# Kernel optimization log

Measured on AMD Instinct MI355X. Metric: run time of the kernel, lower is better.

Reference implementation:

```python
import jax, jax.numpy as jnp
import numpy as np

B, S, HID = 2, 1024, 2048
HQ, HKV, HD = 32, 8, 64
ROPE_BASE = 10000.0

def _rope_tables(seq_len, head_dim):
    inv_freq = 1.0 / (ROPE_BASE ** (np.arange(0, head_dim, 2, dtype=np.float32) / head_dim))
    t = np.arange(seq_len, dtype=np.float32)
    freqs = np.outer(t, inv_freq)                      # [S, d/2]
    emb = np.concatenate([freqs, freqs], axis=-1)      # [S, d]
    return jnp.asarray(np.cos(emb)), jnp.asarray(np.sin(emb))

def setup_inputs() -> dict:
    key = jax.random.key(0)
    ks = jax.random.split(key, 5)
    cos, sin = _rope_tables(S, HD)
    return {
        'hidden_states': jax.random.normal(ks[0], (B, S, HID), jnp.float32),
        'cos': cos, 'sin': sin,
        'Wq': jax.random.normal(ks[1], (HID, HID), jnp.float32) * (HID ** -0.5),
        'Wk': jax.random.normal(ks[2], (HID, HKV * HD), jnp.float32) * (HID ** -0.5),
        'Wv': jax.random.normal(ks[3], (HID, HKV * HD), jnp.float32) * (HID ** -0.5),
        'Wo': jax.random.normal(ks[4], (HID, HID), jnp.float32) * (HID ** -0.5),
    }

def _rotate_half(x):
    d = x.shape[-1]
    return jnp.concatenate([-x[..., d // 2:], x[..., :d // 2]], axis=-1)

def reference(hidden_states, cos, sin, Wq, Wk, Wv, Wo):
    b, s, _ = hidden_states.shape
    q = (hidden_states @ Wq).reshape(b, s, HQ, HD)    # [b,s,Hq,d]
    k = (hidden_states @ Wk).reshape(b, s, HKV, HD)   # [b,s,Hkv,d]
    v = (hidden_states @ Wv).reshape(b, s, HKV, HD)
    # RoPE: cos/sin [s,d] broadcast as [s,1,d] over head dim
    c = cos[:, None, :]
    sn = sin[:, None, :]
    q = q * c + _rotate_half(q) * sn
    k = k * c + _rotate_half(k) * sn
    # GQA: expand kv heads to query heads (repeat_kv)
    n_rep = HQ // HKV
    k = jnp.repeat(k, n_rep, axis=2)                  # [b,s,Hq,d]
    v = jnp.repeat(v, n_rep, axis=2)
    scale = HD ** -0.5
    scores = jnp.einsum('bqhd,bkhd->bhqk', q, k) * scale  # [b,Hq,s,s]
    causal = jnp.tril(jnp.ones((s, s), bool))
    scores = jnp.where(causal, scores, jnp.float32(-1e30))
    probs = jax.nn.softmax(scores.astype(jnp.float32), axis=-1).astype(q.dtype)
    out = jnp.einsum('bhqk,bkhd->bqhd', probs, v).reshape(b, s, HID)
    return out @ Wo
```

## Files before the change

### kernel.cpp

```cpp
#include <hip/hip_runtime.h>
#include <math.h>

#define B_   2
#define S_   1024
#define HID_ 2048
#define HQ_  32
#define HKV_ 8
#define HD_  64
#define NQKV 3072

using short8  = __attribute__((ext_vector_type(8))) short;
using floatx4 = __attribute__((ext_vector_type(4))) float;

__device__ __forceinline__ unsigned short f2bf(float x) {
    unsigned int u = __builtin_bit_cast(unsigned int, x);
    u += 0x7FFFu + ((u >> 16) & 1u);
    return (unsigned short)(u >> 16);
}
__device__ __forceinline__ float bf2f(unsigned short u) {
    return __builtin_bit_cast(float, (unsigned int)u << 16);
}

__device__ __forceinline__ void gl_lds16(const unsigned short* g, unsigned short* l) {
    __builtin_amdgcn_global_load_lds(
        (const __attribute__((address_space(1))) void*)g,
        (__attribute__((address_space(3))) void*)l, 16, 0, 0);
}

__global__ __launch_bounds__(256) void gemm_qkv(const unsigned short* __restrict__ A,
                                                const unsigned short* __restrict__ Bt,
                                                unsigned short* __restrict__ Qp,
                                                unsigned short* __restrict__ KVp) {
    __shared__ __align__(16) unsigned short As[128 * 32];
    __shared__ __align__(16) unsigned short Bs[128 * 32];

    int bid = blockIdx.x;
    int m0, n0, z, Nw, nc0;
    unsigned short* C;
    if (bid < 512) {
        n0 = (bid & 15) * 128; m0 = ((bid >> 4) & 15) * 128; z = bid >> 8;
        C = Qp + (size_t)z * 2048 * 2048; Nw = 2048; nc0 = n0;
    } else {
        bid -= 512;
        n0 = 2048 + (bid & 7) * 128; m0 = ((bid >> 3) & 15) * 128; z = bid >> 7;
        C = KVp + (size_t)z * 2048 * 1024; Nw = 1024; nc0 = n0 - 2048;
    }
    const int kbase = z * 1024;

    const int tid  = threadIdx.x;
    const int w    = tid >> 6;
    const int lane = tid & 63;
    const int col  = lane & 15;
    const int quad = lane >> 4;
    const int wm = (w >> 1) * 64;
    const int wn = (w & 1) * 64;

    const int srow = lane >> 2;
    const int skof = (lane & 3) * 8;
    const unsigned short* Ag = A  + (size_t)(m0 + srow) * HID_ + skof;
    const unsigned short* Bg = Bt + (size_t)(n0 + srow) * HID_ + skof;
    const int rb = w * 16;

    floatx4 acc[4][4] = {};

    for (int k0 = kbase; k0 < kbase + 1024; k0 += 32) {
        gl_lds16(Ag + (size_t)(rb     ) * HID_ + k0, &As[(rb     ) * 32]);
        gl_lds16(Ag + (size_t)(rb + 64) * HID_ + k0, &As[(rb + 64) * 32]);
        gl_lds16(Bg + (size_t)(rb     ) * HID_ + k0, &Bs[(rb     ) * 32]);
        gl_lds16(Bg + (size_t)(rb + 64) * HID_ + k0, &Bs[(rb + 64) * 32]);
        __syncthreads();

        short8 af[4], bfr[4];
#pragma unroll
        for (int i = 0; i < 4; ++i)
            af[i] = *(const short8*)&As[(wm + i * 16 + col) * 32 + quad * 8];
#pragma unroll
        for (int j = 0; j < 4; ++j)
            bfr[j] = *(const short8*)&Bs[(wn + j * 16 + col) * 32 + quad * 8];
#pragma unroll
        for (int i = 0; i < 4; ++i)
#pragma unroll
            for (int j = 0; j < 4; ++j)
                acc[i][j] = __builtin_amdgcn_mfma_f32_16x16x32_bf16(
                    af[i], bfr[j], acc[i][j], 0, 0, 0);
        __syncthreads();
    }

#pragma unroll
    for (int i = 0; i < 4; ++i)
#pragma unroll
        for (int j = 0; j < 4; ++j)
#pragma unroll
            for (int r = 0; r < 4; ++r)
                C[(size_t)(m0 + wm + i * 16 + quad * 4 + r) * Nw
                  + (nc0 + wn + j * 16 + col)] = f2bf(acc[i][j][r]);
}

__global__ __launch_bounds__(256) void gemm_wo(const unsigned short* __restrict__ A,
                                               const unsigned short* __restrict__ Bt,
                                               float* __restrict__ Cf,
                                               unsigned short* __restrict__ Cp1) {
    __shared__ __align__(16) unsigned short As[128 * 32];
    __shared__ __align__(16) unsigned short Bs[128 * 32];

    const int m0 = blockIdx.y * 128;
    const int n0 = blockIdx.x * 128;
    const int z  = blockIdx.z;
    const int kbase = z * 1024;

    const int tid  = threadIdx.x;
    const int w    = tid >> 6;
    const int lane = tid & 63;
    const int col  = lane & 15;
    const int quad = lane >> 4;
    const int wm = (w >> 1) * 64;
    const int wn = (w & 1) * 64;

    const int srow = lane >> 2;
    const int skof = (lane & 3) * 8;
    const unsigned short* Ag = A  + (size_t)(m0 + srow) * HID_ + skof;
    const unsigned short* Bg = Bt + (size_t)(n0 + srow) * HID_ + skof;
    const int rb = w * 16;

    floatx4 acc[4][4] = {};

    for (int k0 = kbase; k0 < kbase + 1024; k0 += 32) {
        gl_lds16(Ag + (size_t)(rb     ) * HID_ + k0, &As[(rb     ) * 32]);
        gl_lds16(Ag + (size_t)(rb + 64) * HID_ + k0, &As[(rb + 64) * 32]);
        gl_lds16(Bg + (size_t)(rb     ) * HID_ + k0, &Bs[(rb     ) * 32]);
        gl_lds16(Bg + (size_t)(rb + 64) * HID_ + k0, &Bs[(rb + 64) * 32]);
        __syncthreads();

        short8 af[4], bfr[4];
#pragma unroll
        for (int i = 0; i < 4; ++i)
            af[i] = *(const short8*)&As[(wm + i * 16 + col) * 32 + quad * 8];
#pragma unroll
        for (int j = 0; j < 4; ++j)
            bfr[j] = *(const short8*)&Bs[(wn + j * 16 + col) * 32 + quad * 8];
#pragma unroll
        for (int i = 0; i < 4; ++i)
#pragma unroll
            for (int j = 0; j < 4; ++j)
                acc[i][j] = __builtin_amdgcn_mfma_f32_16x16x32_bf16(
                    af[i], bfr[j], acc[i][j], 0, 0, 0);
        __syncthreads();
    }

#pragma unroll
    for (int i = 0; i < 4; ++i)
#pragma unroll
        for (int j = 0; j < 4; ++j)
#pragma unroll
            for (int r = 0; r < 4; ++r) {
                size_t off = (size_t)(m0 + wm + i * 16 + quad * 4 + r) * HID_
                           + (n0 + wn + j * 16 + col);
                if (z == 0) Cf[off] = acc[i][j][r];
                else        Cp1[off] = f2bf(acc[i][j][r]);
            }
}

__global__ __launch_bounds__(256) void reduce_wo(float* __restrict__ out,
                                                 const unsigned short* __restrict__ p1) {
    int i4 = (blockIdx.x * 256 + threadIdx.x) * 4;
    float4 o = *(float4*)&out[i4];
    ushort4 p = *(const ushort4*)&p1[i4];
    o.x += bf2f(p.x); o.y += bf2f(p.y); o.z += bf2f(p.z); o.w += bf2f(p.w);
    *(float4*)&out[i4] = o;
}

__global__ __launch_bounds__(256) void convert_x(const float* __restrict__ in,
                                                 unsigned short* __restrict__ out) {
    int tid = blockIdx.x * 256 + threadIdx.x;
    float4 v = *(const float4*)&in[(size_t)tid * 4];
    ushort4 o = {f2bf(v.x), f2bf(v.y), f2bf(v.z), f2bf(v.w)};
    *(ushort4*)&out[(size_t)tid * 4] = o;
}

__global__ __launch_bounds__(256) void transpose_qkv(const float* __restrict__ Wq,
                                                     const float* __restrict__ Wk,
                                                     const float* __restrict__ Wv,
                                                     unsigned short* __restrict__ WcatT) {
    __shared__ float tile[32][33];
    int bid = blockIdx.x;
    const float* W;
    unsigned short* WT;
    int N, tn0, tk0;
    if (bid < 4096) {
        W = Wq; WT = WcatT; N = HID_;
        tn0 = (bid & 63) * 32; tk0 = (bid >> 6) * 32;
    } else if (bid < 5120) {
        bid -= 4096;
        W = Wk; WT = WcatT + (size_t)HID_ * HID_; N = 512;
        tn0 = (bid & 15) * 32; tk0 = (bid >> 4) * 32;
    } else {
        bid -= 5120;
        W = Wv; WT = WcatT + (size_t)(HID_ + 512) * HID_; N = 512;
        tn0 = (bid & 15) * 32; tk0 = (bid >> 4) * 32;
    }
    const int r  = threadIdx.x >> 3;
    const int c4 = (threadIdx.x & 7) * 4;
    float4 v = *(const float4*)&W[(size_t)(tk0 + r) * N + tn0 + c4];
    tile[r][c4 + 0] = v.x;
    tile[r][c4 + 1] = v.y;
    tile[r][c4 + 2] = v.z;
    tile[r][c4 + 3] = v.w;
    __syncthreads();
    ushort4 o = {f2bf(tile[c4 + 0][r]), f2bf(tile[c4 + 1][r]),
                 f2bf(tile[c4 + 2][r]), f2bf(tile[c4 + 3][r])};
    *(ushort4*)&WT[(size_t)(tn0 + r) * HID_ + tk0 + c4] = o;
}

__global__ __launch_bounds__(256) void transpose_wo(const float* __restrict__ Wo,
                                                    unsigned short* __restrict__ WoT) {
    __shared__ float tile[32][33];
    int bid = blockIdx.x;
    const int tn0 = (bid & 63) * 32;
    const int tk0 = (bid >> 6) * 32;
    const int r  = threadIdx.x >> 3;
    const int c4 = (threadIdx.x & 7) * 4;
    float4 v = *(const float4*)&Wo[(size_t)(tk0 + r) * HID_ + tn0 + c4];
    tile[r][c4 + 0] = v.x;
    tile[r][c4 + 1] = v.y;
    tile[r][c4 + 2] = v.z;
    tile[r][c4 + 3] = v.w;
    __syncthreads();
    ushort4 o = {f2bf(tile[c4 + 0][r]), f2bf(tile[c4 + 1][r]),
                 f2bf(tile[c4 + 2][r]), f2bf(tile[c4 + 3][r])};
    *(ushort4*)&WoT[(size_t)(tn0 + r) * HID_ + tk0 + c4] = o;
}

__global__ __launch_bounds__(256) void convert_qkv(const unsigned short* __restrict__ Qp,
                                                   const unsigned short* __restrict__ KVp,
                                                   const float* __restrict__ cosT,
                                                   const float* __restrict__ sinT,
                                                   unsigned short* __restrict__ Qbf,
                                                   unsigned short* __restrict__ Kbf,
                                                   unsigned short* __restrict__ Vt) {
    const size_t QSTR  = (size_t)2048 * 2048;
    const size_t KVSTR = (size_t)2048 * 1024;
    int tid = blockIdx.x * 256 + threadIdx.x;
    const int NQ = B_ * S_ * HQ_ * 32;
    const int NK = B_ * S_ * HKV_ * 32;
    if (tid < NQ) {
        int d = tid & 31;
        int h = (tid >> 5) & (HQ_ - 1);
        int s = (tid >> 10) & (S_ - 1);
        int b = tid >> 20;
        const unsigned short* row = Qp + (size_t)(b * S_ + s) * 2048 + h * HD_;
        float x0 = bf2f(row[d])      + bf2f(row[QSTR + d]);
        float x1 = bf2f(row[d + 32]) + bf2f(row[QSTR + d + 32]);
        float c0 = cosT[s * HD_ + d],      s0 = sinT[s * HD_ + d];
        float c1 = cosT[s * HD_ + d + 32], s1 = sinT[s * HD_ + d + 32];
        unsigned short* orow = Qbf + ((size_t)(b * HQ_ + h) * S_ + s) * HD_;
        orow[d]      = f2bf((x0 * c0 - x1 * s0) * 0.125f);
        orow[d + 32] = f2bf((x1 * c1 + x0 * s1) * 0.125f);
    } else if (tid < NQ + NK) {
        tid -= NQ;
        int d  = tid & 31;
        int kv = (tid >> 5) & (HKV_ - 1);
        int s  = (tid >> 8) & (S_ - 1);
        int b  = tid >> 18;
        const unsigned short* row = KVp + (size_t)(b * S_ + s) * 1024 + kv * HD_;
        float x0 = bf2f(row[d])      + bf2f(row[KVSTR + d]);
        float x1 = bf2f(row[d + 32]) + bf2f(row[KVSTR + d + 32]);
        float c0 = cosT[s * HD_ + d],      s0 = sinT[s * HD_ + d];
        float c1 = cosT[s * HD_ + d + 32], s1 = sinT[s * HD_ + d + 32];
        unsigned short* orow = Kbf + ((size_t)(b * HKV_ + kv) * S_ + s) * HD_;
        orow[d]      = f2bf(x0 * c0 - x1 * s0);
        orow[d + 32] = f2bf(x1 * c1 + x0 * s1);
    } else {
        tid -= NQ + NK;
        int s4 = tid & 255;
        int d  = (tid >> 8) & (HD_ - 1);
        int kv = (tid >> 14) & (HKV_ - 1);
        int b  = tid >> 17;
        int s  = s4 * 4;
        const unsigned short* base =
            KVp + ((size_t)(b * S_ + s)) * 1024 + 512 + kv * HD_ + d;
        ushort4 o;
#pragma unroll
        for (int j = 0; j < 4; ++j) {
            float v = bf2f(base[(size_t)j * 1024]) +
                      bf2f(base[KVSTR + (size_t)j * 1024]);
            ((unsigned short*)&o)[j] = f2bf(v);
        }
        *(ushort4*)&Vt[((size_t)(b * HKV_ + kv) * HD_ + d) * S_ + s] = o;
    }
}

__global__ __launch_bounds__(256) void attn_mfma(const unsigned short* __restrict__ Qbf,
                                                 const unsigned short* __restrict__ Kbf,
                                                 const unsigned short* __restrict__ Vt,
                                                 unsigned short* __restrict__ Ctx) {
    const int tq = 31 - blockIdx.x;
    const int kv = blockIdx.y;
    const int b  = blockIdx.z;
    const int w    = threadIdx.x >> 6;
    const int lane = threadIdx.x & 63;
    const int col  = lane & 15;
    const int quad = lane >> 4;

    const int h   = kv * 4 + w;
    const int bh  = b * HQ_ + h;
    const int bkv = b * HKV_ + kv;
    const int qw  = 32 * tq;

    __shared__ __align__(16) unsigned short sK[2][64 * 64];
    __shared__ __align__(16) unsigned short sV[2][64 * 64];
    __shared__ __align__(16) unsigned short sP[4][32 * 72];
    unsigned short* myP = sP[w];

    short8 bq[2][2];
#pragma unroll
    for (int u = 0; u < 2; ++u) {
        const unsigned short* qrow = Qbf + ((size_t)bh * S_ + qw + 16 * u + col) * HD_;
        bq[u][0] = *(const short8*)&qrow[quad * 8];
        bq[u][1] = *(const short8*)&qrow[32 + quad * 8];
    }

    const unsigned short* Kbase = Kbf + (size_t)bkv * S_ * HD_;
    const unsigned short* Vbase = Vt  + (size_t)bkv * HD_ * S_;

    const int sr  = lane >> 3;
    const int ssl = (lane & 7) ^ sr;
    const int r0  = 16 * w;

    floatx4 acc[2][4] = {};
    float m_i[2] = {-1e30f, -1e30f};
    float l_i[2] = {0.f, 0.f};

    const int nsteps = (qw + 95) >> 6;

#pragma unroll
    for (int c = 0; c < 2; ++c) {
        const int row = r0 + 8 * c + sr;
        gl_lds16(Kbase + (size_t)row * HD_ + ssl * 8, &sK[0][(r0 + 8 * c) * 64]);
        gl_lds16(Vbase + (size_t)row * S_ + ssl * 8,  &sV[0][(r0 + 8 * c) * 64]);
    }
    __syncthreads();

    int cur = 0;
    for (int it = 0; it < nsteps; ++it) {
        const int k0 = it * 64;

        if (it + 1 < nsteps) {
            const int kn = k0 + 64;
#pragma unroll
            for (int c = 0; c < 2; ++c) {
                const int row = r0 + 8 * c + sr;
                gl_lds16(Kbase + (size_t)(kn + row) * HD_ + ssl * 8,
                         &sK[cur ^ 1][(r0 + 8 * c) * 64]);
                gl_lds16(Vbase + (size_t)row * S_ + kn + ssl * 8,
                         &sV[cur ^ 1][(r0 + 8 * c) * 64]);
            }
        }

        floatx4 sc[2][4];
        __builtin_amdgcn_s_setprio(1);
#pragma unroll
        for (int tt = 0; tt < 4; ++tt) {
            const int krow = 16 * tt + col;
            const unsigned short* kr = &sK[cur][krow * 64];
            short8 ak0 = *(const short8*)&kr[((quad    ) ^ (krow & 7)) * 8];
            short8 ak1 = *(const short8*)&kr[((quad + 4) ^ (krow & 7)) * 8];
#pragma unroll
            for (int u = 0; u < 2; ++u) {
                floatx4 z = {0.f, 0.f, 0.f, 0.f};
                z = __builtin_amdgcn_mfma_f32_16x16x32_bf16(ak0, bq[u][0], z, 0, 0, 0);
                z = __builtin_amdgcn_mfma_f32_16x16x32_bf16(ak1, bq[u][1], z, 0, 0, 0);
                sc[u][tt] = z;
            }
        }
        __builtin_amdgcn_s_setprio(0);

#pragma unroll
        for (int u = 0; u < 2; ++u) {
            const int qbase = qw + 16 * u;
            const int myq   = qbase + col;
            if (k0 + 63 > qbase) {
#pragma unroll
                for (int tt = 0; tt < 4; ++tt)
#pragma unroll
                    for (int r = 0; r < 4; ++r)
                        if (k0 + 16 * tt + quad * 4 + r > myq) sc[u][tt][r] = -1e30f;
            }
            float vmax = sc[u][0][0];
#pragma unroll
            for (int tt = 0; tt < 4; ++tt)
#pragma unroll
                for (int r = 0; r < 4; ++r)
                    vmax = fmaxf(vmax, sc[u][tt][r]);
            vmax = fmaxf(vmax, __shfl_xor(vmax, 16, 64));
            vmax = fmaxf(vmax, __shfl_xor(vmax, 32, 64));
            const float mnew  = fmaxf(m_i[u], vmax);
            const float alpha = __expf(m_i[u] - mnew);
            m_i[u] = mnew;
            float lsum = 0.f;
#pragma unroll
            for (int tt = 0; tt < 4; ++tt) {
                float p0 = __expf(sc[u][tt][0] - mnew);
                float p1 = __expf(sc[u][tt][1] - mnew);
                float p2 = __expf(sc[u][tt][2] - mnew);
                float p3 = __expf(sc[u][tt][3] - mnew);
                lsum += (p0 + p1) + (p2 + p3);
                ushort4 pk = {f2bf(p0), f2bf(p1), f2bf(p2), f2bf(p3)};
                *(ushort4*)&myP[(16 * u + col) * 72 + 16 * tt + quad * 4] = pk;
            }
            lsum += __shfl_xor(lsum, 16, 64);
            lsum += __shfl_xor(lsum, 32, 64);
            l_i[u] = l_i[u] * alpha + lsum;
            float a_r[4];
#pragma unroll
            for (int r = 0; r < 4; ++r)
                a_r[r] = __shfl(alpha, quad * 4 + r, 64);
#pragma unroll
            for (int nt = 0; nt < 4; ++nt)
#pragma unroll
                for (int r = 0; r < 4; ++r)
                    acc[u][nt][r] *= a_r[r];
        }

        short8 pa[2][2];
#pragma unroll
        for (int u = 0; u < 2; ++u) {
            pa[u][0] = *(const short8*)&myP[(16 * u + col) * 72 + quad * 8];
            pa[u][1] = *(const short8*)&myP[(16 * u + col) * 72 + 32 + quad * 8];
        }
        __builtin_amdgcn_s_setprio(1);
#pragma unroll
        for (int nt = 0; nt < 4; ++nt) {
            const int vrow = 16 * nt + col;
            const unsigned short* vr = &sV[cur][vrow * 64];
            short8 vb0 = *(const short8*)&vr[((quad    ) ^ (vrow & 7)) * 8];
            short8 vb1 = *(const short8*)&vr[((quad + 4) ^ (vrow & 7)) * 8];
#pragma unroll
            for (int u = 0; u < 2; ++u) {
                acc[u][nt] = __builtin_amdgcn_mfma_f32_16x16x32_bf16(pa[u][0], vb0, acc[u][nt], 0, 0, 0);
                acc[u][nt] = __builtin_amdgcn_mfma_f32_16x16x32_bf16(pa[u][1], vb1, acc[u][nt], 0, 0, 0);
            }
        }
        __builtin_amdgcn_s_setprio(0);

        __syncthreads();
        cur ^= 1;
    }

#pragma unroll
    for (int u = 0; u < 2; ++u) {
        const float invl = 1.0f / l_i[u];
        float inv_r[4];
#pragma unroll
        for (int r = 0; r < 4; ++r)
            inv_r[r] = __shfl(invl, quad * 4 + r, 64);
#pragma unroll
        for (int nt = 0; nt < 4; ++nt)
#pragma unroll
            for (int r = 0; r < 4; ++r)
                Ctx[(size_t)(b * S_ + qw + 16 * u + quad * 4 + r) * HID_
                    + h * HD_ + nt * 16 + col] = f2bf(acc[u][nt][r] * inv_r[r]);
    }
}

extern "C" void kernel_launch(void* const* d_in, const int* in_sizes, int n_in,
                              void* d_out, int out_size, void* d_ws, size_t ws_size,
                              hipStream_t stream) {
    const float* X    = (const float*)d_in[0];
    const float* cosT = (const float*)d_in[1];
    const float* sinT = (const float*)d_in[2];
    const float* Wq   = (const float*)d_in[3];
    const float* Wk   = (const float*)d_in[4];
    const float* Wv   = (const float*)d_in[5];
    const float* Wo   = (const float*)d_in[6];

    const int M = B_ * S_;
    const size_t MB = 1024u * 1024u;

    char* ws = (char*)d_ws;
    unsigned short* Xbf   = (unsigned short*)(ws);
    unsigned short* Qbf   = (unsigned short*)(ws);
    unsigned short* WcatT = (unsigned short*)(ws + 8 * MB);
    unsigned short* Kbf   = (unsigned short*)(ws + 8 * MB);
    unsigned short* Vt    = (unsigned short*)(ws + 10 * MB);
    unsigned short* WoT   = (unsigned short*)(ws + 12 * MB);
    unsigned short* KVp   = (unsigned short*)(ws + 20 * MB);
    unsigned short* Ctxbf = (unsigned short*)(ws + 20 * MB);
    unsigned short* Wop1  = (unsigned short*)(ws);
    unsigned short* Qp    = (unsigned short*)d_out;
    float* out = (float*)d_out;

    convert_x<<<(M * HID_ / 4) / 256, 256, 0, stream>>>(X, Xbf);

    transpose_qkv<<<6144, 256, 0, stream>>>(Wq, Wk, Wv, WcatT);

    gemm_qkv<<<768, 256, 0, stream>>>(Xbf, WcatT, Qp, KVp);

    {
        int total = B_ * S_ * HQ_ * 32 + B_ * S_ * HKV_ * 32
                  + B_ * HKV_ * HD_ * (S_ / 4);
        convert_qkv<<<total / 256, 256, 0, stream>>>(Qp, KVp, cosT, sinT,
                                                     Qbf, Kbf, Vt);
    }

    transpose_wo<<<4096, 256, 0, stream>>>(Wo, WoT);

    attn_mfma<<<dim3(32, HKV_, B_), 256, 0, stream>>>(Qbf, Kbf, Vt, Ctxbf);

    gemm_wo<<<dim3(16, 16, 2), 256, 0, stream>>>(Ctxbf, WoT, out, Wop1);

    reduce_wo<<<(M * HID_ / 4) / 256, 256, 0, stream>>>(out, Wop1);
}
```

Before: 245.8 us.

## Load K/V fragments directly from global into registers, drop LDS staging

The attention kernel no longer stages K and V tiles through double-buffered shared memory with block-wide barriers. Each wave loads its own MFMA operand fragments straight from global memory into registers. K is prefetched one step ahead and V is loaded at the start of each step. This removes LDS traffic and the __syncthreads per iteration, but each of the four waves sharing a KV head now fetches the same K/V data separately. It relies on L2/L1 hits and adds register pressure and exposed global-load latency for V.

```diff
diff --git a/kernel.cpp b/kernel.cpp
--- a/kernel.cpp
+++ b/kernel.cpp
@@ -306,8 +306,6 @@
     const int bkv = b * HKV_ + kv;
     const int qw  = 32 * tq;
 
-    __shared__ __align__(16) unsigned short sK[2][64 * 64];
-    __shared__ __align__(16) unsigned short sV[2][64 * 64];
     __shared__ __align__(16) unsigned short sP[4][32 * 72];
     unsigned short* myP = sP[w];
 
@@ -319,12 +317,8 @@
         bq[u][1] = *(const short8*)&qrow[32 + quad * 8];
     }
 
-    const unsigned short* Kbase = Kbf + (size_t)bkv * S_ * HD_;
-    const unsigned short* Vbase = Vt  + (size_t)bkv * HD_ * S_;
-
-    const int sr  = lane >> 3;
-    const int ssl = (lane & 7) ^ sr;
-    const int r0  = 16 * w;
+    const unsigned short* Kl = Kbf + ((size_t)bkv * S_ + col) * HD_ + quad * 8;
+    const unsigned short* Vl = Vt  + ((size_t)bkv * HD_ + col) * S_ + quad * 8;
 
     floatx4 acc[2][4] = {};
     float m_i[2] = {-1e30f, -1e30f};
@@ -332,47 +326,48 @@
 
     const int nsteps = (qw + 95) >> 6;
 
-#pragma unroll
-    for (int c = 0; c < 2; ++c) {
-        const int row = r0 + 8 * c + sr;
-        gl_lds16(Kbase + (size_t)row * HD_ + ssl * 8, &sK[0][(r0 + 8 * c) * 64]);
-        gl_lds16(Vbase + (size_t)row * S_ + ssl * 8,  &sV[0][(r0 + 8 * c) * 64]);
-    }
-    __syncthreads();
-
-    int cur = 0;
+    short8 ka[4][2];
+#pragma unroll
+    for (int tt = 0; tt < 4; ++tt) {
+#pragma unroll
+        for (int hf = 0; hf < 2; ++hf)
+            ka[tt][hf] = *(const short8*)&Kl[(size_t)(16 * tt) * HD_ + hf * 32];
+    }
+
     for (int it = 0; it < nsteps; ++it) {
         const int k0 = it * 64;
 
+        short8 va[4][2];
+#pragma unroll
+        for (int nt = 0; nt < 4; ++nt) {
+#pragma unroll
+            for (int hf = 0; hf < 2; ++hf)
+                va[nt][hf] = *(const short8*)&Vl[(size_t)(16 * nt) * S_ + k0 + hf * 32];
+        }
+
+        floatx4 sc[2][4];
+        __builtin_amdgcn_s_setprio(1);
+#pragma unroll
+        for (int tt = 0; tt < 4; ++tt) {
+#pragma unroll
+            for (int u = 0; u < 2; ++u) {
+                floatx4 z = {0.f, 0.f, 0.f, 0.f};
+                z = __builtin_amdgcn_mfma_f32_16x16x32_bf16(ka[tt][0], bq[u][0], z, 0, 0, 0);
+                z = __builtin_amdgcn_mfma_f32_16x16x32_bf16(ka[tt][1], bq[u][1], z, 0, 0, 0);
+                sc[u][tt] = z;
+            }
+        }
+        __builtin_amdgcn_s_setprio(0);
+
         if (it + 1 < nsteps) {
             const int kn = k0 + 64;
 #pragma unroll
-            for (int c = 0; c < 2; ++c) {
-                const int row = r0 + 8 * c + sr;
-                gl_lds16(Kbase + (size_t)(kn + row) * HD_ + ssl * 8,
-                         &sK[cur ^ 1][(r0 + 8 * c) * 64]);
-                gl_lds16(Vbase + (size_t)row * S_ + kn + ssl * 8,
-                         &sV[cur ^ 1][(r0 + 8 * c) * 64]);
+            for (int tt = 0; tt < 4; ++tt) {
+#pragma unroll
+                for (int hf = 0; hf < 2; ++hf)
+                    ka[tt][hf] = *(const short8*)&Kl[(size_t)(kn + 16 * tt) * HD_ + hf * 32];
             }
         }
-
-        floatx4 sc[2][4];
-        __builtin_amdgcn_s_setprio(1);
-#pragma unroll
-        for (int tt = 0; tt < 4; ++tt) {
-            const int krow = 16 * tt + col;
-            const unsigned short* kr = &sK[cur][krow * 64];
-            short8 ak0 = *(const short8*)&kr[((quad    ) ^ (krow & 7)) * 8];
-            short8 ak1 = *(const short8*)&kr[((quad + 4) ^ (krow & 7)) * 8];
-#pragma unroll
-            for (int u = 0; u < 2; ++u) {
-                floatx4 z = {0.f, 0.f, 0.f, 0.f};
-                z = __builtin_amdgcn_mfma_f32_16x16x32_bf16(ak0, bq[u][0], z, 0, 0, 0);
-                z = __builtin_amdgcn_mfma_f32_16x16x32_bf16(ak1, bq[u][1], z, 0, 0, 0);
-                sc[u][tt] = z;
-            }
-        }
-        __builtin_amdgcn_s_setprio(0);
 
 #pragma unroll
         for (int u = 0; u < 2; ++u) {
@@ -430,20 +425,13 @@
         __builtin_amdgcn_s_setprio(1);
 #pragma unroll
         for (int nt = 0; nt < 4; ++nt) {
-            const int vrow = 16 * nt + col;
-            const unsigned short* vr = &sV[cur][vrow * 64];
-            short8 vb0 = *(const short8*)&vr[((quad    ) ^ (vrow & 7)) * 8];
-            short8 vb1 = *(const short8*)&vr[((quad + 4) ^ (vrow & 7)) * 8];
 #pragma unroll
             for (int u = 0; u < 2; ++u) {
-                acc[u][nt] = __builtin_amdgcn_mfma_f32_16x16x32_bf16(pa[u][0], vb0, acc[u][nt], 0, 0, 0);
-                acc[u][nt] = __builtin_amdgcn_mfma_f32_16x16x32_bf16(pa[u][1], vb1, acc[u][nt], 0, 0, 0);
+                acc[u][nt] = __builtin_amdgcn_mfma_f32_16x16x32_bf16(pa[u][0], va[nt][0], acc[u][nt], 0, 0, 0);
+                acc[u][nt] = __builtin_amdgcn_mfma_f32_16x16x32_bf16(pa[u][1], va[nt][1], acc[u][nt], 0, 0, 0);
             }
         }
         __builtin_amdgcn_s_setprio(0);
-
-        __syncthreads();
-        cur ^= 1;
     }
 
 #pragma unroll
```

New measurement: 264.2 us. 1.07x slower.

## Split long causal query tiles across two KV chunks and merge partials

Applied to the files above, without the earlier changes.

Query tiles in the upper half of the sequence (tq 16..31) now each run as two blocks, and each block covers half of the KV steps. The blocks write unnormalized fp32 partial outputs plus their running max and sum into scratch. A new merge kernel then combines the two halves with a log-sum-exp rescale. The aim is to balance causal work across blocks and raise the block count beyond 512, so the tail from the longest tiles gets shorter. The cost is an extra launch, fp32 scratch traffic through d_out and ws, and a reorder that moves transpose_wo after attention, since its WoT region is reused for the ML buffer.

```diff
diff --git a/kernel.cpp b/kernel.cpp
--- a/kernel.cpp
+++ b/kernel.cpp
@@ -8,6 +8,8 @@
 #define HKV_ 8
 #define HD_  64
 #define NQKV 3072
+
+#define PCHUNK 2097152
 
 using short8  = __attribute__((ext_vector_type(8))) short;
 using floatx4 = __attribute__((ext_vector_type(4))) float;
@@ -292,10 +294,26 @@
 __global__ __launch_bounds__(256) void attn_mfma(const unsigned short* __restrict__ Qbf,
                                                  const unsigned short* __restrict__ Kbf,
                                                  const unsigned short* __restrict__ Vt,
-                                                 unsigned short* __restrict__ Ctx) {
-    const int tq = 31 - blockIdx.x;
+                                                 unsigned short* __restrict__ Ctx,
+                                                 float* __restrict__ PO,
+                                                 float* __restrict__ ML) {
+    const int x  = blockIdx.x;
     const int kv = blockIdx.y;
     const int b  = blockIdx.z;
+
+    int tq, chunk, it0, it1;
+    if (x < 32) {
+        tq = 16 + (x >> 1); chunk = x & 1;
+        const int ns = (32 * tq + 95) >> 6;
+        const int hh = ns >> 1;
+        it0 = chunk ? hh : 0;
+        it1 = chunk ? ns : hh;
+    } else {
+        tq = 47 - x; chunk = -1;
+        it0 = 0;
+        it1 = (32 * tq + 95) >> 6;
+    }
+
     const int w    = threadIdx.x >> 6;
     const int lane = threadIdx.x & 63;
     const int col  = lane & 15;
@@ -330,21 +348,22 @@
     float m_i[2] = {-1e30f, -1e30f};
     float l_i[2] = {0.f, 0.f};
 
-    const int nsteps = (qw + 95) >> 6;
-
-#pragma unroll
-    for (int c = 0; c < 2; ++c) {
-        const int row = r0 + 8 * c + sr;
-        gl_lds16(Kbase + (size_t)row * HD_ + ssl * 8, &sK[0][(r0 + 8 * c) * 64]);
-        gl_lds16(Vbase + (size_t)row * S_ + ssl * 8,  &sV[0][(r0 + 8 * c) * 64]);
+    {
+        const int kb = it0 * 64;
+#pragma unroll
+        for (int c = 0; c < 2; ++c) {
+            const int row = r0 + 8 * c + sr;
+            gl_lds16(Kbase + (size_t)(kb + row) * HD_ + ssl * 8, &sK[0][(r0 + 8 * c) * 64]);
+            gl_lds16(Vbase + (size_t)row * S_ + kb + ssl * 8,    &sV[0][(r0 + 8 * c) * 64]);
+        }
     }
     __syncthreads();
 
     int cur = 0;
-    for (int it = 0; it < nsteps; ++it) {
+    for (int it = it0; it < it1; ++it) {
         const int k0 = it * 64;
 
-        if (it + 1 < nsteps) {
+        if (it + 1 < it1) {
             const int kn = k0 + 64;
 #pragma unroll
             for (int c = 0; c < 2; ++c) {
@@ -446,20 +465,78 @@
         cur ^= 1;
     }
 
-#pragma unroll
-    for (int u = 0; u < 2; ++u) {
-        const float invl = 1.0f / l_i[u];
-        float inv_r[4];
-#pragma unroll
-        for (int r = 0; r < 4; ++r)
-            inv_r[r] = __shfl(invl, quad * 4 + r, 64);
-#pragma unroll
-        for (int nt = 0; nt < 4; ++nt)
+    if (chunk < 0) {
+#pragma unroll
+        for (int u = 0; u < 2; ++u) {
+            const float invl = 1.0f / l_i[u];
+            float inv_r[4];
 #pragma unroll
             for (int r = 0; r < 4; ++r)
-                Ctx[(size_t)(b * S_ + qw + 16 * u + quad * 4 + r) * HID_
-                    + h * HD_ + nt * 16 + col] = f2bf(acc[u][nt][r] * inv_r[r]);
-    }
+                inv_r[r] = __shfl(invl, quad * 4 + r, 64);
+#pragma unroll
+            for (int nt = 0; nt < 4; ++nt)
+#pragma unroll
+                for (int r = 0; r < 4; ++r)
+                    Ctx[(size_t)(b * S_ + qw + 16 * u + quad * 4 + r) * HID_
+                        + h * HD_ + nt * 16 + col] = f2bf(acc[u][nt][r] * inv_r[r]);
+        }
+    } else {
+        const int ts = tq - 16;
+        const int base_row = (((b * 8 + kv) * 16 + ts) * 4 + w) * 32;
+        float* POc = PO + (size_t)chunk * PCHUNK;
+#pragma unroll
+        for (int u = 0; u < 2; ++u)
+#pragma unroll
+            for (int nt = 0; nt < 4; ++nt)
+#pragma unroll
+                for (int r = 0; r < 4; ++r)
+                    POc[(size_t)(base_row + 16 * u + quad * 4 + r) * 64
+                        + nt * 16 + col] = acc[u][nt][r];
+        if (quad == 0) {
+#pragma unroll
+            for (int u = 0; u < 2; ++u) {
+                const int rr = chunk * 32768 + base_row + 16 * u + col;
+                ML[rr * 2 + 0] = m_i[u];
+                ML[rr * 2 + 1] = l_i[u];
+            }
+        }
+    }
+}
+
+__global__ __launch_bounds__(256) void merge_attn(const float* __restrict__ PO,
+                                                  const float* __restrict__ ML,
+                                                  unsigned short* __restrict__ Ctx) {
+    const int tid = blockIdx.x * 256 + threadIdx.x;
+    const int i4  = tid * 4;
+    const int row = i4 >> 6;
+    const int d0  = i4 & 63;
+
+    const float m0 = ML[row * 2 + 0];
+    const float l0 = ML[row * 2 + 1];
+    const float m1 = ML[(32768 + row) * 2 + 0];
+    const float l1 = ML[(32768 + row) * 2 + 1];
+    const float mf = fmaxf(m0, m1);
+    const float s0 = __expf(m0 - mf);
+    const float s1 = __expf(m1 - mf);
+    const float inv = 1.0f / (l0 * s0 + l1 * s1);
+
+    float4 o0 = *(const float4*)&PO[(size_t)row * 64 + d0];
+    float4 o1 = *(const float4*)&PO[(size_t)PCHUNK + (size_t)row * 64 + d0];
+
+    const int q  = row & 31;
+    const int hh = (row >> 5) & 3;
+    const int ts = (row >> 7) & 15;
+    const int kv = (row >> 11) & 7;
+    const int b  = row >> 14;
+    const int q_abs = 512 + ts * 32 + q;
+    const int h_abs = kv * 4 + hh;
+
+    ushort4 o;
+    o.x = f2bf((o0.x * s0 + o1.x * s1) * inv);
+    o.y = f2bf((o0.y * s0 + o1.y * s1) * inv);
+    o.z = f2bf((o0.z * s0 + o1.z * s1) * inv);
+    o.w = f2bf((o0.w * s0 + o1.w * s1) * inv);
+    *(ushort4*)&Ctx[((size_t)(b * S_ + q_abs)) * HID_ + h_abs * HD_ + d0] = o;
 }
 
 extern "C" void kernel_launch(void* const* d_in, const int* in_sizes, int n_in,
@@ -482,11 +559,13 @@
     unsigned short* WcatT = (unsigned short*)(ws + 8 * MB);
     unsigned short* Kbf   = (unsigned short*)(ws + 8 * MB);
     unsigned short* Vt    = (unsigned short*)(ws + 10 * MB);
+    float*          MLb   = (float*)(ws + 12 * MB);
     unsigned short* WoT   = (unsigned short*)(ws + 12 * MB);
     unsigned short* KVp   = (unsigned short*)(ws + 20 * MB);
     unsigned short* Ctxbf = (unsigned short*)(ws + 20 * MB);
     unsigned short* Wop1  = (unsigned short*)(ws);
     unsigned short* Qp    = (unsigned short*)d_out;
+    float*          PO    = (float*)d_out;
     float* out = (float*)d_out;
 
     convert_x<<<(M * HID_ / 4) / 256, 256, 0, stream>>>(X, Xbf);
@@ -502,10 +581,13 @@
                                                      Qbf, Kbf, Vt);
     }
 
+    attn_mfma<<<dim3(48, HKV_, B_), 256, 0, stream>>>(Qbf, Kbf, Vt, Ctxbf,
+                                                      PO, MLb);
+
+    merge_attn<<<2048, 256, 0, stream>>>(PO, MLb, Ctxbf);
+
     transpose_wo<<<4096, 256, 0, stream>>>(Wo, WoT);
 
-    attn_mfma<<<dim3(32, HKV_, B_), 256, 0, stream>>>(Qbf, Kbf, Vt, Ctxbf);
-
     gemm_wo<<<dim3(16, 16, 2), 256, 0, stream>>>(Ctxbf, WoT, out, Wop1);
 
     reduce_wo<<<(M * HID_ / 4) / 256, 256, 0, stream>>>(out, Wop1);
```

New measurement: 246.1 us. About the same (+0.1%).
